# Kernel tuning notes

Hardware: AMD Instinct MI355X
Metric: run time of the kernel (lower is better)

Reference implementation:

```python
import jax, jax.numpy as jnp
import numpy as np

ROWS, D_IN, UNITS = 8192, 4096, 4096
CLIP_VAL = 100.0
THRESH = 0.5  # SteTern threshold


def ternarize(w):
    # SteTern(0.5): +1 if w > 0.5, -1 if w < -0.5, else 0
    return jnp.where(w > THRESH, 1.0, jnp.where(w < -THRESH, -1.0, 0.0)).astype(w.dtype)


def setup_inputs() -> dict:
    key = jax.random.key(0)
    k1, k2 = jax.random.split(key)
    x = jax.random.normal(k1, (ROWS, D_IN), dtype=jnp.float32)
    W = jax.random.normal(k2, (D_IN, UNITS), dtype=jnp.float32)
    scale = jnp.ones((UNITS,), dtype=jnp.float32)
    bias = jnp.zeros((UNITS,), dtype=jnp.float32)
    return {"x": x, "W": W, "scale": scale, "bias": bias}


def reference(x, W, scale, bias):
    wq = ternarize(W)                       # [D_IN, UNITS] in {-1,0,+1}
    y = jnp.matmul(x, wq)                   # [ROWS, UNITS]
    y = y * scale + bias
    y = jnp.clip(y, -CLIP_VAL, CLIP_VAL)
    return y
```

## Files before the change

### kernel.cpp

```cpp
#include <hip/hip_runtime.h>
#include <hip/hip_bf16.h>
#include <stdint.h>

namespace {

constexpr int M = 8192;
constexpr int N = 4096;
constexpr int K = 4096;
constexpr float CLIP = 100.0f;
constexpr float THRESH = 0.5f;

typedef __bf16 bf16x8 __attribute__((ext_vector_type(8)));
typedef __bf16 bf16x4 __attribute__((ext_vector_type(4)));
typedef float f32x4 __attribute__((ext_vector_type(4)));

__device__ __forceinline__ void load16_to_lds(const void* gptr, void* lptr) {
  __builtin_amdgcn_global_load_lds(
      (const __attribute__((address_space(1))) uint32_t*)gptr,
      (__attribute__((address_space(3))) uint32_t*)lptr,
      16, 0, 0);
}

__device__ __forceinline__ __bf16 tern(float w) {
  return (__bf16)((w > THRESH) ? 1.0f : ((w < -THRESH) ? -1.0f : 0.0f));
}

__global__ __launch_bounds__(256) void prep_x_kernel(
    const float* __restrict__ x, __bf16* __restrict__ xb) {
  const int total = M * K / 8;
  const int stride = gridDim.x * blockDim.x;
  for (int i = blockIdx.x * blockDim.x + threadIdx.x; i < total; i += stride) {
    const float4 v0 = reinterpret_cast<const float4*>(x)[2 * i];
    const float4 v1 = reinterpret_cast<const float4*>(x)[2 * i + 1];
    bf16x8 c;
    c[0] = (__bf16)v0.x; c[1] = (__bf16)v0.y; c[2] = (__bf16)v0.z; c[3] = (__bf16)v0.w;
    c[4] = (__bf16)v1.x; c[5] = (__bf16)v1.y; c[6] = (__bf16)v1.z; c[7] = (__bf16)v1.w;
    reinterpret_cast<bf16x8*>(xb)[i] = c;
  }
}

__global__ __launch_bounds__(256) void prep_w_kernel(
    const float* __restrict__ W, __bf16* __restrict__ Wt) {
  __shared__ __bf16 sT[64][68];
  const int t = threadIdx.x;
  const int k0 = blockIdx.y * 64;
  const int n0 = blockIdx.x * 64;

#pragma unroll
  for (int i = 0; i < 4; ++i) {
    const int k = i * 16 + (t >> 4);
    const int n4 = (t & 15);
    const float4 v = *reinterpret_cast<const float4*>(
        W + (size_t)(k0 + k) * N + n0 + n4 * 4);
    bf16x4 c;
    c[0] = tern(v.x); c[1] = tern(v.y); c[2] = tern(v.z); c[3] = tern(v.w);
    *reinterpret_cast<bf16x4*>(&sT[k][n4 * 4]) = c;
  }
  __syncthreads();
#pragma unroll
  for (int i = 0; i < 4; ++i) {
    const int n = i * 16 + (t >> 4);
    const int k4 = (t & 15);
    bf16x4 c;
#pragma unroll
    for (int cc = 0; cc < 4; ++cc) c[cc] = sT[k4 * 4 + cc][n];
    *reinterpret_cast<bf16x4*>(Wt + (size_t)(n0 + n) * K + k0 + k4 * 4) = c;
  }
}

constexpr int BK = 64;
constexpr int REG_BYTES = 16384;
constexpr int BUF_BYTES = 4 * REG_BYTES;

__device__ __forceinline__ int swz(int x) { return x ^ (((x >> 7) & 3) << 4); }

#define PH_SYNC()                                        \
  do {                                                   \
    __builtin_amdgcn_s_barrier();                        \
    asm volatile("s_waitcnt lgkmcnt(0)" ::: "memory");   \
    __builtin_amdgcn_sched_barrier(0);                   \
  } while (0)

#define PH_MFMA(ro)                                      \
  do {                                                   \
    __builtin_amdgcn_s_setprio(1);                       \
    mfma_block(ro);                                      \
    __builtin_amdgcn_s_setprio(0);                       \
    __builtin_amdgcn_sched_barrier(0);                   \
    __builtin_amdgcn_s_barrier();                        \
  } while (0)

#define PH_MFMA_VM(ro, n)                                \
  do {                                                   \
    __builtin_amdgcn_s_setprio(1);                       \
    mfma_block(ro);                                      \
    __builtin_amdgcn_s_setprio(0);                       \
    asm volatile("s_waitcnt vmcnt(" #n ")" ::: "memory");\
    __builtin_amdgcn_sched_barrier(0);                   \
    __builtin_amdgcn_s_barrier();                        \
  } while (0)

__global__ __launch_bounds__(512, 2) void gemm256_kernel(
    const __bf16* __restrict__ A, const __bf16* __restrict__ Bt,
    const float* __restrict__ scale, const float* __restrict__ bias,
    float* __restrict__ out) {
  __shared__ __attribute__((aligned(16))) char lds[2 * BUF_BYTES];

  const int tid  = threadIdx.x;
  const int lane = tid & 63;
  const int w    = tid >> 6;
  const int wrow = w >> 2;
  const int wcol = w & 3;
  const int l15  = lane & 15;
  const int quad = lane >> 4;

  int bid = blockIdx.x;
  bid = (bid & 7) * 64 + (bid >> 3);
  const int bm = (bid >> 4) * 256;
  const int bn = (bid & 15) * 256;

  int st_dst[2];
  const __bf16* a_src[2];
  const __bf16* b_src[2];
#pragma unroll
  for (int c = 0; c < 2; ++c) {
    const int p  = w * 1024 + c * 8192 + lane * 16;
    const int lg = swz(p);
    const int row  = lg >> 6;
    const int colb = lg & 63;
    st_dst[c] = w * 1024 + c * 8192;
    a_src[c] = A  + (size_t)(bm + row) * K + (colb >> 1);
    b_src[c] = Bt + (size_t)(bn + row) * K + (colb >> 1);
  }

  auto stageA = [&](int buf, int h, int k0) {
#pragma unroll
    for (int c = 0; c < 2; ++c)
      load16_to_lds(a_src[c] + k0 + h * 32,
                    &lds[buf * BUF_BYTES + h * REG_BYTES + st_dst[c]]);
  };
  auto stageB = [&](int buf, int h, int k0) {
#pragma unroll
    for (int c = 0; c < 2; ++c)
      load16_to_lds(b_src[c] + k0 + h * 32,
                    &lds[buf * BUF_BYTES + (2 + h) * REG_BYTES + st_dst[c]]);
  };

  int aoff[8], boff[4];
#pragma unroll
  for (int i = 0; i < 8; ++i) {
    const int row = wrow * 128 + i * 16 + l15;
    aoff[i] = swz(row * 64 + quad * 16);
  }
#pragma unroll
  for (int j = 0; j < 4; ++j) {
    const int row = wcol * 64 + j * 16 + l15;
    boff[j] = swz(row * 64 + quad * 16);
  }

  f32x4 acc[8][4] = {};
  bf16x8 aF[4], bF[4];

  auto rdA4 = [&](int buf, int ks, int i0) {
#pragma unroll
    for (int i = 0; i < 4; ++i)
      aF[i] = *reinterpret_cast<const bf16x8*>(
          &lds[buf * BUF_BYTES + ks * REG_BYTES + aoff[i0 + i]]);
  };
  auto rdB4 = [&](int buf, int ks) {
#pragma unroll
    for (int j = 0; j < 4; ++j)
      bF[j] = *reinterpret_cast<const bf16x8*>(
          &lds[buf * BUF_BYTES + (2 + ks) * REG_BYTES + boff[j]]);
  };
  auto mfma_block = [&](int ro) {
#pragma unroll
    for (int i = 0; i < 4; ++i)
#pragma unroll
      for (int j = 0; j < 4; ++j)
        acc[ro + i][j] = __builtin_amdgcn_mfma_f32_16x16x32_bf16(
            aF[i], bF[j], acc[ro + i][j], 0, 0, 0);
  };

  stageA(0, 0, 0);
  stageB(0, 0, 0);
  stageA(0, 1, 0);
  stageB(0, 1, 0);
  stageB(1, 0, BK);
  stageA(1, 0, BK);
  stageB(1, 1, BK);
  asm volatile("s_waitcnt vmcnt(6)" ::: "memory");
  __builtin_amdgcn_sched_barrier(0);
  __builtin_amdgcn_s_barrier();

  for (int k2 = 0; k2 + 2 * BK < K; k2 += 2 * BK) {
    const int kO  = k2 + BK;
    const int kE2 = k2 + 2 * BK;
    const int kO2 = k2 + 3 * BK;
    rdA4(0, 0, 0); rdB4(0, 0);
    stageA(1, 1, kO);
    PH_SYNC(); PH_MFMA(0);
    rdA4(0, 0, 4);
    stageB(0, 0, kE2);
    PH_SYNC(); PH_MFMA(4);
    rdA4(0, 1, 0); rdB4(0, 1);
    stageA(0, 0, kE2);
    PH_SYNC(); PH_MFMA(0);
    rdA4(0, 1, 4);
    stageB(0, 1, kE2);
    PH_SYNC(); PH_MFMA_VM(4, 6);
    rdA4(1, 0, 0); rdB4(1, 0);
    stageA(0, 1, kE2);
    PH_SYNC(); PH_MFMA(0);
    rdA4(1, 0, 4);
    stageB(1, 0, kO2);
    PH_SYNC(); PH_MFMA(4);
    rdA4(1, 1, 0); rdB4(1, 1);
    stageA(1, 0, kO2);
    PH_SYNC(); PH_MFMA(0);
    rdA4(1, 1, 4);
    stageB(1, 1, kO2);
    PH_SYNC(); PH_MFMA_VM(4, 6);
  }

  stageA(1, 1, K - BK);
  rdA4(0, 0, 0); rdB4(0, 0); PH_SYNC(); PH_MFMA(0);
  rdA4(0, 0, 4);             PH_SYNC(); PH_MFMA(4);
  rdA4(0, 1, 0); rdB4(0, 1); PH_SYNC(); PH_MFMA(0);
  rdA4(0, 1, 4);             PH_SYNC(); PH_MFMA_VM(4, 0);
  rdA4(1, 0, 0); rdB4(1, 0); PH_SYNC(); PH_MFMA(0);
  rdA4(1, 0, 4);             PH_SYNC(); PH_MFMA(4);
  rdA4(1, 1, 0); rdB4(1, 1); PH_SYNC(); PH_MFMA(0);
  rdA4(1, 1, 4);             PH_SYNC(); PH_MFMA(4);

#pragma unroll
  for (int j = 0; j < 4; ++j) {
    const int n = bn + wcol * 64 + j * 16 + l15;
    const float s = scale[n];
    const float b = bias[n];
#pragma unroll
    for (int i = 0; i < 8; ++i) {
#pragma unroll
      for (int r = 0; r < 4; ++r) {
        const int m = bm + wrow * 128 + i * 16 + quad * 4 + r;
        float v = acc[i][j][r] * s + b;
        v = fminf(fmaxf(v, -CLIP), CLIP);
        out[(size_t)m * N + n] = v;
      }
    }
  }
}

constexpr int LDA = 40;
constexpr int LDB = 40;

__global__ __launch_bounds__(256) void ternary_gemm_fallback(
    const float* __restrict__ x, const float* __restrict__ W,
    const float* __restrict__ scale, const float* __restrict__ bias,
    float* __restrict__ out) {
  __shared__ __bf16 sA[128 * LDA];
  __shared__ __bf16 sB[128 * LDB];

  const int tid  = threadIdx.x;
  const int lane = tid & 63;
  const int wave = tid >> 6;
  const int wm   = (wave >> 1) * 64;
  const int wn   = (wave & 1) * 64;
  const int l15  = lane & 15;
  const int quad = lane >> 4;
  const int bm = blockIdx.y * 128;
  const int bn = blockIdx.x * 128;
  const int a_row = tid >> 3;
  const int a_c4  = tid & 7;
  const int b_kg = tid >> 5;
  const int b_ng = tid & 31;

  f32x4 acc[4][4] = {};
  for (int k0 = 0; k0 < K; k0 += 32) {
#pragma unroll
    for (int i = 0; i < 4; ++i) {
      const int row = a_row + i * 32;
      const float4 v = *reinterpret_cast<const float4*>(
          x + (size_t)(bm + row) * K + k0 + a_c4 * 4);
      bf16x4 c;
      c[0] = (__bf16)v.x; c[1] = (__bf16)v.y; c[2] = (__bf16)v.z; c[3] = (__bf16)v.w;
      *reinterpret_cast<bf16x4*>(&sA[row * LDA + a_c4 * 4]) = c;
    }
    {
      __bf16 t[4][4];
#pragma unroll
      for (int j = 0; j < 4; ++j) {
        const float4 v = *reinterpret_cast<const float4*>(
            W + (size_t)(k0 + b_kg * 4 + j) * N + bn + b_ng * 4);
        t[j][0] = tern(v.x); t[j][1] = tern(v.y); t[j][2] = tern(v.z); t[j][3] = tern(v.w);
      }
#pragma unroll
      for (int c = 0; c < 4; ++c) {
        bf16x4 col;
        col[0] = t[0][c]; col[1] = t[1][c]; col[2] = t[2][c]; col[3] = t[3][c];
        *reinterpret_cast<bf16x4*>(&sB[(b_ng * 4 + c) * LDB + b_kg * 4]) = col;
      }
    }
    __syncthreads();
    bf16x8 af[4], bfr[4];
#pragma unroll
    for (int i = 0; i < 4; ++i)
      af[i] = *reinterpret_cast<const bf16x8*>(&sA[(wm + i * 16 + l15) * LDA + quad * 8]);
#pragma unroll
    for (int j = 0; j < 4; ++j)
      bfr[j] = *reinterpret_cast<const bf16x8*>(&sB[(wn + j * 16 + l15) * LDB + quad * 8]);
#pragma unroll
    for (int i = 0; i < 4; ++i)
#pragma unroll
      for (int j = 0; j < 4; ++j)
        acc[i][j] = __builtin_amdgcn_mfma_f32_16x16x32_bf16(af[i], bfr[j], acc[i][j], 0, 0, 0);
    __syncthreads();
  }
#pragma unroll
  for (int j = 0; j < 4; ++j) {
    const int n = bn + wn + j * 16 + l15;
    const float s = scale[n];
    const float b = bias[n];
#pragma unroll
    for (int i = 0; i < 4; ++i)
#pragma unroll
      for (int r = 0; r < 4; ++r) {
        const int m = bm + wm + i * 16 + quad * 4 + r;
        float v = acc[i][j][r] * s + b;
        v = fminf(fmaxf(v, -CLIP), CLIP);
        out[(size_t)m * N + n] = v;
      }
  }
}

}

extern "C" void kernel_launch(void* const* d_in, const int* in_sizes, int n_in,
                              void* d_out, int out_size, void* d_ws, size_t ws_size,
                              hipStream_t stream) {
  const float* x     = (const float*)d_in[0];
  const float* W     = (const float*)d_in[1];
  const float* scale = (const float*)d_in[2];
  const float* bias  = (const float*)d_in[3];
  float* out = (float*)d_out;

  const size_t xb_bytes = (size_t)M * K * sizeof(__bf16);
  const size_t wt_bytes = (size_t)N * K * sizeof(__bf16);

  if (ws_size >= xb_bytes + wt_bytes) {
    __bf16* xb = (__bf16*)d_ws;
    __bf16* wt = (__bf16*)((char*)d_ws + xb_bytes);
    prep_x_kernel<<<2048, 256, 0, stream>>>(x, xb);
    prep_w_kernel<<<dim3(N / 64, K / 64), 256, 0, stream>>>(W, wt);
    gemm256_kernel<<<dim3((M / 256) * (N / 256)), 512, 0, stream>>>(xb, wt, scale, bias, out);
  } else {
    ternary_gemm_fallback<<<dim3(N / 128, M / 128), 256, 0, stream>>>(x, W, scale, bias, out);
  }
}
```

Measured before the change: 493.4 us.

## Merge prep kernels into one launch and stage GEMM epilogue through LDS

The x bf16-cast and W ternarize-transpose kernels become a single launch, with blocks split by index, which saves one launch and lets the two passes run side by side. The GEMM epilogue now writes scaled and clipped results into per-wave LDS scratch. It then reads them back as 16-byte row-contiguous vectors and stores them with nontemporal stores, replacing the scattered 4-byte column stores. This adds a __syncthreads and extra LDS traffic, and it relies on the LDS buffer being free to reuse after the main loop.

```diff
diff --git a/kernel.cpp b/kernel.cpp
--- a/kernel.cpp
+++ b/kernel.cpp
@@ -25,46 +25,48 @@
   return (__bf16)((w > THRESH) ? 1.0f : ((w < -THRESH) ? -1.0f : 0.0f));
 }
 
-__global__ __launch_bounds__(256) void prep_x_kernel(
-    const float* __restrict__ x, __bf16* __restrict__ xb) {
-  const int total = M * K / 8;
-  const int stride = gridDim.x * blockDim.x;
-  for (int i = blockIdx.x * blockDim.x + threadIdx.x; i < total; i += stride) {
-    const float4 v0 = reinterpret_cast<const float4*>(x)[2 * i];
-    const float4 v1 = reinterpret_cast<const float4*>(x)[2 * i + 1];
-    bf16x8 c;
-    c[0] = (__bf16)v0.x; c[1] = (__bf16)v0.y; c[2] = (__bf16)v0.z; c[3] = (__bf16)v0.w;
-    c[4] = (__bf16)v1.x; c[5] = (__bf16)v1.y; c[6] = (__bf16)v1.z; c[7] = (__bf16)v1.w;
-    reinterpret_cast<bf16x8*>(xb)[i] = c;
-  }
-}
-
-__global__ __launch_bounds__(256) void prep_w_kernel(
+__global__ __launch_bounds__(256) void prep_fused_kernel(
+    const float* __restrict__ x, __bf16* __restrict__ xb,
     const float* __restrict__ W, __bf16* __restrict__ Wt) {
   __shared__ __bf16 sT[64][68];
-  const int t = threadIdx.x;
-  const int k0 = blockIdx.y * 64;
-  const int n0 = blockIdx.x * 64;
-
-#pragma unroll
-  for (int i = 0; i < 4; ++i) {
-    const int k = i * 16 + (t >> 4);
-    const int n4 = (t & 15);
-    const float4 v = *reinterpret_cast<const float4*>(
-        W + (size_t)(k0 + k) * N + n0 + n4 * 4);
-    bf16x4 c;
-    c[0] = tern(v.x); c[1] = tern(v.y); c[2] = tern(v.z); c[3] = tern(v.w);
-    *reinterpret_cast<bf16x4*>(&sT[k][n4 * 4]) = c;
-  }
-  __syncthreads();
-#pragma unroll
-  for (int i = 0; i < 4; ++i) {
-    const int n = i * 16 + (t >> 4);
-    const int k4 = (t & 15);
-    bf16x4 c;
-#pragma unroll
-    for (int cc = 0; cc < 4; ++cc) c[cc] = sT[k4 * 4 + cc][n];
-    *reinterpret_cast<bf16x4*>(Wt + (size_t)(n0 + n) * K + k0 + k4 * 4) = c;
+
+  if (blockIdx.x < 2048) {
+    const int total = M * K / 8;
+    const int stride = 2048 * 256;
+    for (int i = blockIdx.x * 256 + threadIdx.x; i < total; i += stride) {
+      const float4 v0 = reinterpret_cast<const float4*>(x)[2 * i];
+      const float4 v1 = reinterpret_cast<const float4*>(x)[2 * i + 1];
+      bf16x8 c;
+      c[0] = (__bf16)v0.x; c[1] = (__bf16)v0.y; c[2] = (__bf16)v0.z; c[3] = (__bf16)v0.w;
+      c[4] = (__bf16)v1.x; c[5] = (__bf16)v1.y; c[6] = (__bf16)v1.z; c[7] = (__bf16)v1.w;
+      reinterpret_cast<bf16x8*>(xb)[i] = c;
+    }
+  } else {
+    const int wb = blockIdx.x - 2048;
+    const int t = threadIdx.x;
+    const int n0 = (wb & 63) * 64;
+    const int k0 = (wb >> 6) * 64;
+
+#pragma unroll
+    for (int i = 0; i < 4; ++i) {
+      const int k = i * 16 + (t >> 4);
+      const int n4 = (t & 15);
+      const float4 v = *reinterpret_cast<const float4*>(
+          W + (size_t)(k0 + k) * N + n0 + n4 * 4);
+      bf16x4 c;
+      c[0] = tern(v.x); c[1] = tern(v.y); c[2] = tern(v.z); c[3] = tern(v.w);
+      *reinterpret_cast<bf16x4*>(&sT[k][n4 * 4]) = c;
+    }
+    __syncthreads();
+#pragma unroll
+    for (int i = 0; i < 4; ++i) {
+      const int n = i * 16 + (t >> 4);
+      const int k4 = (t & 15);
+      bf16x4 c;
+#pragma unroll
+      for (int cc = 0; cc < 4; ++cc) c[cc] = sT[k4 * 4 + cc][n];
+      *reinterpret_cast<bf16x4*>(Wt + (size_t)(n0 + n) * K + k0 + k4 * 4) = c;
+    }
   }
 }
 
@@ -233,20 +235,39 @@
   rdA4(1, 1, 0); rdB4(1, 1); PH_SYNC(); PH_MFMA(0);
   rdA4(1, 1, 4);             PH_SYNC(); PH_MFMA(4);
 
+  __syncthreads();
+
+  float* cbuf = reinterpret_cast<float*>(&lds[w * 16384]);
+  const int baseM = bm + wrow * 128;
+  const int baseN = bn + wcol * 64;
+  float sv[4], bv[4];
 #pragma unroll
   for (int j = 0; j < 4; ++j) {
-    const int n = bn + wcol * 64 + j * 16 + l15;
-    const float s = scale[n];
-    const float b = bias[n];
-#pragma unroll
-    for (int i = 0; i < 8; ++i) {
-#pragma unroll
-      for (int r = 0; r < 4; ++r) {
-        const int m = bm + wrow * 128 + i * 16 + quad * 4 + r;
-        float v = acc[i][j][r] * s + b;
-        v = fminf(fmaxf(v, -CLIP), CLIP);
-        out[(size_t)m * N + n] = v;
+    sv[j] = scale[baseN + j * 16 + l15];
+    bv[j] = bias[baseN + j * 16 + l15];
+  }
+#pragma unroll
+  for (int h = 0; h < 2; ++h) {
+#pragma unroll
+    for (int i = 0; i < 4; ++i) {
+      const int ii = h * 4 + i;
+#pragma unroll
+      for (int j = 0; j < 4; ++j) {
+#pragma unroll
+        for (int r = 0; r < 4; ++r) {
+          float v = acc[ii][j][r] * sv[j] + bv[j];
+          v = fminf(fmaxf(v, -CLIP), CLIP);
+          cbuf[(i * 16 + quad * 4 + r) * 64 + j * 16 + l15] = v;
+        }
       }
+    }
+#pragma unroll
+    for (int g = 0; g < 16; ++g) {
+      const int row = g * 4 + quad;
+      const f32x4 v = *reinterpret_cast<const f32x4*>(&cbuf[row * 64 + l15 * 4]);
+      __builtin_nontemporal_store(
+          v, reinterpret_cast<f32x4*>(out + (size_t)(baseM + h * 64 + row) * N +
+                                      baseN + l15 * 4));
     }
   }
 }
@@ -350,8 +371,7 @@
   if (ws_size >= xb_bytes + wt_bytes) {
     __bf16* xb = (__bf16*)d_ws;
     __bf16* wt = (__bf16*)((char*)d_ws + xb_bytes);
-    prep_x_kernel<<<2048, 256, 0, stream>>>(x, xb);
-    prep_w_kernel<<<dim3(N / 64, K / 64), 256, 0, stream>>>(W, wt);
+    prep_fused_kernel<<<6144, 256, 0, stream>>>(x, xb, W, wt);
     gemm256_kernel<<<dim3((M / 256) * (N / 256)), 512, 0, stream>>>(xb, wt, scale, bias, out);
   } else {
     ternary_gemm_fallback<<<dim3(N / 128, M / 128), 256, 0, stream>>>(x, W, scale, bias, out);
```

Measured after the change: 481.7 us. 2.4% less time.
